# Kernel optimization log

Hardware: AMD Instinct MI355X
Metric: run time of the kernel (lower is better)

Reference implementation:

```python
import jax, jax.numpy as jnp
import numpy as np

L0, L1, L2 = 32, 16, 8          # multiplicities of 0e, 1o, 2e irreps
NS = 128                        # numscalars
NB = 64                         # numbasis
CUTOFF = 7.0
N_NODES = 50000
N_EDGES = 400000
N_GRAPH = 32
NODE_DIM = L0 + 3 * L1 + 5 * L2  # 120


def setup_inputs() -> dict:
    key = jax.random.key(0)
    ks = jax.random.split(key, 16)
    return {
        "nodes": jax.random.normal(ks[0], (N_NODES, NODE_DIM), jnp.float32),
        "edge_index": jax.random.randint(ks[1], (2, N_EDGES), 0, N_NODES),
        "graph_batch": jnp.sort(jax.random.randint(ks[2], (N_NODES,), 0, N_GRAPH)),
        "cell": jax.random.normal(ks[3], (N_GRAPH, 3, 3), jnp.float32),
        "edge_shift": jax.random.normal(ks[4], (N_EDGES, 3), jnp.float32),
        "pos": jax.random.normal(ks[5], (N_NODES, 3), jnp.float32),
        # FullyConnectedTensorProduct weights: one uvw block per (l,l)->0e path
        "W0": jax.random.normal(ks[6], (L0, L0, NS), jnp.float32),
        "W1": jax.random.normal(ks[7], (L1, L1, NS), jnp.float32),
        "W2": jax.random.normal(ks[8], (L2, L2, NS), jnp.float32),
        "ln_g": jnp.ones((NS,), jnp.float32),
        "ln_b": jnp.zeros((NS,), jnp.float32),
        "df_w1": jax.random.normal(ks[9], (NB, 128), jnp.float32) / np.sqrt(NB).astype(np.float32),
        "df_b1": jnp.zeros((128,), jnp.float32),
        "df_w2": jax.random.normal(ks[10], (128, NS), jnp.float32) / np.sqrt(128.0).astype(np.float32),
        "df_b2": jnp.zeros((NS,), jnp.float32),
        "mlp_w1": jax.random.normal(ks[11], (NS, 512), jnp.float32) / np.sqrt(NS).astype(np.float32),
        "mlp_b1": jnp.zeros((512,), jnp.float32),
        "mlp_w2": jax.random.normal(ks[12], (512, 1), jnp.float32) / np.sqrt(512.0).astype(np.float32),
        "mlp_b2": jnp.zeros((1,), jnp.float32),
    }


def _split_irreps(x):
    # x: [E, L0 + 3*L1 + 5*L2] -> scalar / vector / rank-2 blocks
    a = x[:, :L0]                                   # [E, L0]    0e
    b = x[:, L0:L0 + 3 * L1].reshape(-1, L1, 3)     # [E, L1, 3] 1o
    c = x[:, L0 + 3 * L1:].reshape(-1, L2, 5)       # [E, L2, 5] 2e
    return a, b, c


def _tensor_product(x1, x2, W0, W1, W2):
    # e3nn FullyConnectedTensorProduct to {NS}x0e: only (l,l)->0 paths survive.
    # Real-basis wigner_3j(l,l,0) = I / sqrt(2l+1); 'element' path norm with
    # scalar output gives alpha = 1 / (L0^2 + L1^2 + L2^2) shared by all paths.
    a1, b1, c1 = _split_irreps(x1)
    a2, b2, c2 = _split_irreps(x2)
    alpha = 1.0 / np.sqrt(float(L0 * L0 + L1 * L1 + L2 * L2))
    out = (jnp.einsum('eu,ev,uvw->ew', a1, a2, W0)
           + jnp.einsum('eum,evm,uvw->ew', b1, b2, W1) * (1.0 / np.sqrt(3.0))
           + jnp.einsum('eum,evm,uvw->ew', c1, c2, W2) * (1.0 / np.sqrt(5.0)))
    return jnp.asarray(alpha, out.dtype) * out


def reference(nodes, edge_index, graph_batch, cell, edge_shift, pos,
              W0, W1, W2, ln_g, ln_b, df_w1, df_b1, df_w2, df_b2,
              mlp_w1, mlp_b1, mlp_w2, mlp_b2):
    src, dst = edge_index[0], edge_index[1]
    bcell = cell[graph_batch[src]]                            # [E,3,3]
    tvec = jnp.einsum('ei,eij->ej', edge_shift, bcell)        # [E,3]
    radvec = pos[dst] - pos[src] + tvec
    dist = jnp.linalg.norm(radvec, axis=1, keepdims=True)     # [E,1]

    mixed = _tensor_product(nodes[src], nodes[dst], W0, W1, W2)  # [E,NS]
    mu = jnp.mean(mixed, axis=-1, keepdims=True)
    var = jnp.mean((mixed - mu) ** 2, axis=-1, keepdims=True)
    mixednorm = (mixed - mu) / jnp.sqrt(var + 1e-5) * ln_g + ln_b

    # RadialEmbedding: Gaussian RBF * cosine envelope with hard cutoff
    offset = jnp.linspace(0.0, CUTOFF, NB).astype(dist.dtype)
    width = CUTOFF / (NB - 1)
    coeff = -0.5 / (width * width)
    rbf = jnp.exp(coeff * (dist - offset[None, :]) ** 2)      # [E,NB]
    env = 0.5 * (jnp.cos(dist * jnp.pi / CUTOFF) + 1.0)
    env = env * (dist < CUTOFF).astype(dist.dtype)            # [E,1]
    demb = rbf * env

    dfilter = jax.nn.silu(demb @ df_w1 + df_b1) @ df_w2 + df_b2  # [E,NS]
    regulated = mixednorm * dfilter
    out = jax.nn.silu(regulated @ mlp_w1 + mlp_b1) @ mlp_w2 + mlp_b2  # [E,1]
    return out
```

## Files before the change

kernel.cpp:

```cpp
#include <hip/hip_runtime.h>
#include <hip/hip_bf16.h>
#include <math.h>

typedef unsigned short ushort_t;
typedef short short8 __attribute__((ext_vector_type(8)));
typedef float f32x4 __attribute__((ext_vector_type(4)));

#define E_TOTAL 400000
#define ET 64
#define NTHR 512
#define NODE_D 120
#define ASTR 36
#define BCSTR 92

#define ALPHA 0.0272772362793f
#define S_L1  0.57735026918962f
#define S_L2  0.44721359549996f

#define WS_WF1 172032
#define WS_WF2 180224
#define WS_WM1 196608
#define WS_TOTAL 262144

__device__ __forceinline__ ushort_t f2b(float f) {
    unsigned int b = __float_as_uint(f);
    b += 0x7FFFu + ((b >> 16) & 1u);
    return (ushort_t)(b >> 16);
}
__device__ __forceinline__ unsigned int f2b2(float a, float b) {
    __hip_bfloat162 h = __float22bfloat162_rn(make_float2(a, b));
    union { __hip_bfloat162 h2; unsigned int u; } cv; cv.h2 = h;
    return cv.u;
}
__device__ __forceinline__ float silu_f(float x) { return x / (1.0f + __expf(-x)); }

__global__ __launch_bounds__(256) void prep_weights(
    const float* __restrict__ W0, const float* __restrict__ W1, const float* __restrict__ W2,
    const float* __restrict__ df_w1, const float* __restrict__ df_w2,
    const float* __restrict__ mlp_w1, ushort_t* __restrict__ ws)
{
    const int i = blockIdx.x * 256 + threadIdx.x;
    if (i >= WS_TOTAL) return;
    float v;
    if (i < WS_WF1) {
        const int r = i;
        const int kt = r >> 12, nt = (r >> 9) & 7, l = (r >> 3) & 63, jj = r & 7;
        const int k = kt * 32 + ((l >> 4) << 3) + jj;
        const int n = nt * 16 + (l & 15);
        if (k < 1024)      v = W0[k * 128 + n] * ALPHA;
        else if (k < 1280) v = W1[(k - 1024) * 128 + n] * (ALPHA * S_L1);
        else               v = W2[(k - 1280) * 128 + n] * (ALPHA * S_L2);
    } else if (i < WS_WF2) {
        const int r = i - WS_WF1;
        const int kt = r >> 12, nt = (r >> 9) & 7, l = (r >> 3) & 63, jj = r & 7;
        v = df_w1[(kt * 32 + ((l >> 4) << 3) + jj) * 128 + nt * 16 + (l & 15)];
    } else if (i < WS_WM1) {
        const int r = i - WS_WF2;
        const int kt = r >> 12, nt = (r >> 9) & 7, l = (r >> 3) & 63, jj = r & 7;
        v = df_w2[(kt * 32 + ((l >> 4) << 3) + jj) * 128 + nt * 16 + (l & 15)];
    } else {
        const int r = i - WS_WM1;
        const int kt = r >> 14, nt = (r >> 9) & 31, l = (r >> 3) & 63, jj = r & 7;
        v = mlp_w1[(kt * 32 + ((l >> 4) << 3) + jj) * 512 + nt * 16 + (l & 15)];
    }
    ws[i] = f2b(v);
}

__global__ __launch_bounds__(NTHR, 4) void fused_edge_kernel(
    const float* __restrict__ nodes, const int* __restrict__ edge_index,
    const int* __restrict__ graph_batch, const float* __restrict__ cell,
    const float* __restrict__ edge_shift, const float* __restrict__ pos,
    const float* __restrict__ ln_g, const float* __restrict__ ln_b,
    const float* __restrict__ df_b1, const float* __restrict__ df_b2,
    const float* __restrict__ mlp_b1, const float* __restrict__ mlp_w2,
    const float* __restrict__ mlp_b2,
    const ushort_t* __restrict__ wsp, float* __restrict__ out)
{
    __shared__ __align__(16) ushort_t Pf[8 * 4 * 64 * 8];
    __shared__ __align__(16) char Xb[47104];
    __shared__ float dist_s[ET];
    __shared__ int sidx[ET], didx[ET];
    __shared__ float mu_s[ET], rstd_s[ET];

    float* xa1 = (float*)Xb;
    float* xa2 = xa1 + ET * ASTR;
    float* bc1 = (float*)Xb;
    float* bc2 = bc1 + ET * BCSTR;
    ushort_t* h1F  = (ushort_t*)Xb;
    ushort_t* regF = h1F + 8192;
    float* red1 = (float*)(Xb + 32768);
    float* red2 = (float*)(Xb + 36864);
    ushort_t* dembF = Pf + 4096;

    const int tid = threadIdx.x;
    const int e0g = blockIdx.x * ET;
    const int wave = tid >> 6, lane = tid & 63;
    const int lr = lane & 15, lg = lane >> 4;
    const int er = tid & 15, kg = (tid >> 4) & 3, w = tid >> 6;

    if (tid < ET) {
        const int e = e0g + tid;
        const int s = edge_index[e];
        const int d = edge_index[E_TOTAL + e];
        sidx[tid] = s; didx[tid] = d;
        const int g = graph_batch[s];
        const float* c = cell + g * 9;
        const float sx = edge_shift[e * 3], sy = edge_shift[e * 3 + 1], sz = edge_shift[e * 3 + 2];
        const float t0 = sx * c[0] + sy * c[3] + sz * c[6];
        const float t1 = sx * c[1] + sy * c[4] + sz * c[7];
        const float t2 = sx * c[2] + sy * c[5] + sz * c[8];
        const float r0 = pos[d * 3 + 0] - pos[s * 3 + 0] + t0;
        const float r1 = pos[d * 3 + 1] - pos[s * 3 + 1] + t1;
        const float r2 = pos[d * 3 + 2] - pos[s * 3 + 2] + t2;
        dist_s[tid] = sqrtf(r0 * r0 + r1 * r1 + r2 * r2);
    }
    __syncthreads();

    {
        const int e = tid >> 3, c = tid & 7;
        *(float4*)(xa1 + e * ASTR + c * 4) = *(const float4*)(nodes + (size_t)sidx[e] * NODE_D + c * 4);
        *(float4*)(xa2 + e * ASTR + c * 4) = *(const float4*)(nodes + (size_t)didx[e] * NODE_D + c * 4);
    }
    __syncthreads();

    const char* pA = (const char*)Pf + lane * 16;
    const short8* WT8 = (const short8*)wsp;
    const int bcol = tid;

    f32x4 acc[4] = {{0.f,0.f,0.f,0.f},{0.f,0.f,0.f,0.f},{0.f,0.f,0.f,0.f},{0.f,0.f,0.f,0.f}};

    float2 a2v[4][4];
#pragma unroll
    for (int h = 0; h < 4; ++h)
#pragma unroll
        for (int q = 0; q < 4; ++q)
            a2v[h][q] = *(const float2*)(xa2 + (h * 16 + er) * ASTR + kg * 8 + q * 2);

#pragma unroll 1
    for (int c4 = 0; c4 < 4; ++c4) {
#pragma unroll
        for (int h = 0; h < 4; ++h) {
            const float a1 = xa1[(h * 16 + er) * ASTR + c4 * 8 + w];
            uint4 o;
            o.x = f2b2(a1 * a2v[h][0].x, a1 * a2v[h][0].y);
            o.y = f2b2(a1 * a2v[h][1].x, a1 * a2v[h][1].y);
            o.z = f2b2(a1 * a2v[h][2].x, a1 * a2v[h][2].y);
            o.w = f2b2(a1 * a2v[h][3].x, a1 * a2v[h][3].y);
            *(uint4*)(Pf + ((w * 4 + h) * 64 + kg * 16 + er) * 8) = o;
        }
        __syncthreads();
#pragma unroll 2
        for (int kt = 0; kt < 8; ++kt) {
            const short8 b = WT8[(c4 * 8 + kt) * 512 + bcol];
#pragma unroll
            for (int h = 0; h < 4; ++h) {
                const short8 a = *(const short8*)(pA + (kt * 4 + h) * 1024);
                acc[h] = __builtin_amdgcn_mfma_f32_16x16x32_bf16(a, b, acc[h], 0, 0, 0);
            }
        }
        if (c4 == 3) {
            for (int i = tid; i < ET * 22; i += NTHR) {
                const int e = i / 22, c = i % 22;
                *(float4*)(bc1 + e * BCSTR + c * 4) =
                    *(const float4*)(nodes + (size_t)sidx[e] * NODE_D + 32 + c * 4);
            }
            for (int i = tid; i < ET * 22; i += NTHR) {
                const int e = i / 22, c = i % 22;
                *(float4*)(bc2 + e * BCSTR + c * 4) =
                    *(const float4*)(nodes + (size_t)didx[e] * NODE_D + 32 + c * 4);
            }
        }
        __syncthreads();
    }

    {
        const int u1 = 2 * w + (kg >> 1);
        const int vb = (kg & 1) * 8;
#pragma unroll
        for (int h = 0; h < 4; ++h) {
            const int e = h * 16 + er;
            const float* b1p = bc1 + e * BCSTR + 3 * u1;
            const float b1a = b1p[0], b1b = b1p[1], b1c = b1p[2];
            const float* b2b = bc2 + e * BCSTR + 3 * vb;
            float pr[8];
#pragma unroll
            for (int jj = 0; jj < 8; ++jj) {
                const float* b2p = b2b + 3 * jj;
                pr[jj] = b1a * b2p[0] + b1b * b2p[1] + b1c * b2p[2];
            }
            uint4 o;
            o.x = f2b2(pr[0], pr[1]); o.y = f2b2(pr[2], pr[3]);
            o.z = f2b2(pr[4], pr[5]); o.w = f2b2(pr[6], pr[7]);
            *(uint4*)(Pf + ((w * 4 + h) * 64 + kg * 16 + er) * 8) = o;
        }
    }
    __syncthreads();
#pragma unroll 2
    for (int kt = 0; kt < 8; ++kt) {
        const short8 b = WT8[(32 + kt) * 512 + bcol];
#pragma unroll
        for (int h = 0; h < 4; ++h) {
            const short8 a = *(const short8*)(pA + (kt * 4 + h) * 1024);
            acc[h] = __builtin_amdgcn_mfma_f32_16x16x32_bf16(a, b, acc[h], 0, 0, 0);
        }
    }
    __syncthreads();

    {
        const int ktl = w >> 2, h2 = w & 3;
        const int u2 = ktl * 4 + kg;
        const int e = h2 * 16 + er;
        const float* c1p = bc1 + e * BCSTR + 48 + 5 * u2;
        const float c1a = c1p[0], c1b = c1p[1], c1c = c1p[2], c1d = c1p[3], c1e = c1p[4];
        float pr[8];
#pragma unroll
        for (int jj = 0; jj < 8; ++jj) {
            const float* c2p = bc2 + e * BCSTR + 48 + 5 * jj;
            pr[jj] = c1a * c2p[0] + c1b * c2p[1] + c1c * c2p[2] + c1d * c2p[3] + c1e * c2p[4];
        }
        uint4 o;
        o.x = f2b2(pr[0], pr[1]); o.y = f2b2(pr[2], pr[3]);
        o.z = f2b2(pr[4], pr[5]); o.w = f2b2(pr[6], pr[7]);
        *(uint4*)(Pf + ((ktl * 4 + h2) * 64 + kg * 16 + er) * 8) = o;
    }
    __syncthreads();
#pragma unroll
    for (int kt = 0; kt < 2; ++kt) {
        const short8 b = WT8[(40 + kt) * 512 + bcol];
#pragma unroll
        for (int h = 0; h < 4; ++h) {
            const short8 a = *(const short8*)(pA + (kt * 4 + h) * 1024);
            acc[h] = __builtin_amdgcn_mfma_f32_16x16x32_bf16(a, b, acc[h], 0, 0, 0);
        }
    }
    for (int i = tid; i < ET * 64; i += NTHR) {
        const int e = i >> 6, k = i & 63;
        const float d = dist_s[e];
        const float t = d - (7.0f / 63.0f) * (float)k;
        const float rbf = __expf(-40.5f * t * t);
        const float env = (d < 7.0f) ? (0.5f * (__cosf(d * (3.14159265358979f / 7.0f)) + 1.0f)) : 0.0f;
        const int ktl = k >> 5, kgd = (k >> 3) & 3, jj = k & 7, half = e >> 4, row = e & 15;
        dembF[((ktl * 4 + half) * 64 + kgd * 16 + row) * 8 + jj] = f2b(rbf * env);
    }
    __syncthreads();

    {
        f32x4 f[4] = {{0.f,0.f,0.f,0.f},{0.f,0.f,0.f,0.f},{0.f,0.f,0.f,0.f},{0.f,0.f,0.f,0.f}};
        const char* dA = (const char*)dembF + lane * 16;
#pragma unroll
        for (int kt = 0; kt < 2; ++kt) {
            const short8 b = WT8[WS_WF1 / 8 + kt * 512 + bcol];
#pragma unroll
            for (int h = 0; h < 4; ++h) {
                const short8 a = *(const short8*)(dA + (kt * 4 + h) * 1024);
                f[h] = __builtin_amdgcn_mfma_f32_16x16x32_bf16(a, b, f[h], 0, 0, 0);
            }
        }
        const int n = wave * 16 + lr;
        const float bb = df_b1[n];
        const int ktl = n >> 5, kg2 = (n >> 3) & 3, jjn = n & 7;
#pragma unroll
        for (int h = 0; h < 4; ++h)
#pragma unroll
            for (int r = 0; r < 4; ++r)
                h1F[((ktl * 4 + h) * 64 + kg2 * 16 + lg * 4 + r) * 8 + jjn] = f2b(silu_f(f[h][r] + bb));
    }
    __syncthreads();

    f32x4 d[4] = {{0.f,0.f,0.f,0.f},{0.f,0.f,0.f,0.f},{0.f,0.f,0.f,0.f},{0.f,0.f,0.f,0.f}};
    {
        const char* hA = (const char*)h1F + lane * 16;
#pragma unroll
        for (int kt = 0; kt < 4; ++kt) {
            const short8 b = WT8[WS_WF2 / 8 + kt * 512 + bcol];
#pragma unroll
            for (int h = 0; h < 4; ++h) {
                const short8 a = *(const short8*)(hA + (kt * 4 + h) * 1024);
                d[h] = __builtin_amdgcn_mfma_f32_16x16x32_bf16(a, b, d[h], 0, 0, 0);
            }
        }
        const int n = wave * 16 + lr;
        const float b2v = df_b2[n];
#pragma unroll
        for (int h = 0; h < 4; ++h)
#pragma unroll
            for (int r = 0; r < 4; ++r) d[h][r] += b2v;
    }
#pragma unroll
    for (int h = 0; h < 4; ++h) {
#pragma unroll
        for (int r = 0; r < 4; ++r) {
            const float v = acc[h][r];
            float s1 = v, s2 = v * v;
            s1 += __shfl_xor(s1, 1);  s2 += __shfl_xor(s2, 1);
            s1 += __shfl_xor(s1, 2);  s2 += __shfl_xor(s2, 2);
            s1 += __shfl_xor(s1, 4);  s2 += __shfl_xor(s2, 4);
            s1 += __shfl_xor(s1, 8);  s2 += __shfl_xor(s2, 8);
            if (lr == 0) {
                const int idx = ((wave * 4 + h) * 4 + lg) * 4 + r;
                red1[idx] = s1;
                red1[512 + idx] = s2;
            }
        }
    }
    __syncthreads();
    if (tid < ET) {
        const int h = tid >> 4, g = (tid >> 2) & 3, r = tid & 3;
        float s1 = 0.f, s2 = 0.f;
#pragma unroll
        for (int ww = 0; ww < 8; ++ww) {
            const int idx = ((ww * 4 + h) * 4 + g) * 4 + r;
            s1 += red1[idx];
            s2 += red1[512 + idx];
        }
        const float mu = s1 * (1.0f / 128.0f);
        const float var = s2 * (1.0f / 128.0f) - mu * mu;
        mu_s[tid] = mu;
        rstd_s[tid] = rsqrtf(var + 1e-5f);
    }
    __syncthreads();

    {
        const int n = wave * 16 + lr;
        const float gv = ln_g[n], bv = ln_b[n];
        const int ktl = n >> 5, kg2 = (n >> 3) & 3, jjn = n & 7;
#pragma unroll
        for (int h = 0; h < 4; ++h) {
#pragma unroll
            for (int r = 0; r < 4; ++r) {
                const int row = lg * 4 + r, e = h * 16 + row;
                const float ln = (acc[h][r] - mu_s[e]) * rstd_s[e] * gv + bv;
                regF[((ktl * 4 + h) * 64 + kg2 * 16 + row) * 8 + jjn] = f2b(ln * d[h][r]);
            }
        }
    }
    __syncthreads();

    {
        f32x4 m[4][4];
#pragma unroll
        for (int q = 0; q < 4; ++q)
#pragma unroll
            for (int h = 0; h < 4; ++h) m[q][h] = (f32x4){0.f,0.f,0.f,0.f};
        const char* rA = (const char*)regF + lane * 16;
#pragma unroll
        for (int kt = 0; kt < 4; ++kt) {
            short8 a[4];
#pragma unroll
            for (int h = 0; h < 4; ++h)
                a[h] = *(const short8*)(rA + (kt * 4 + h) * 1024);
            const int base = WS_WM1 / 8 + kt * 2048 + wave * 256 + lane;
#pragma unroll
            for (int q = 0; q < 4; ++q) {
                const short8 b = WT8[base + q * 64];
#pragma unroll
                for (int h = 0; h < 4; ++h)
                    m[q][h] = __builtin_amdgcn_mfma_f32_16x16x32_bf16(a[h], b, m[q][h], 0, 0, 0);
            }
        }
        float po[4][4];
#pragma unroll
        for (int h = 0; h < 4; ++h)
#pragma unroll
            for (int r = 0; r < 4; ++r) po[h][r] = 0.f;
#pragma unroll
        for (int q = 0; q < 4; ++q) {
            const int n = (wave * 4 + q) * 16 + lr;
            const float b1v = mlp_b1[n];
            const float w2v = mlp_w2[n];
#pragma unroll
            for (int h = 0; h < 4; ++h)
#pragma unroll
                for (int r = 0; r < 4; ++r)
                    po[h][r] += silu_f(m[q][h][r] + b1v) * w2v;
        }
#pragma unroll
        for (int h = 0; h < 4; ++h) {
#pragma unroll
            for (int r = 0; r < 4; ++r) {
                float a = po[h][r];
                a += __shfl_xor(a, 1);
                a += __shfl_xor(a, 2);
                a += __shfl_xor(a, 4);
                a += __shfl_xor(a, 8);
                if (lr == 0) red2[((wave * 4 + h) * 4 + lg) * 4 + r] = a;
            }
        }
    }
    __syncthreads();
    if (tid < ET) {
        const int h = tid >> 4, g = (tid >> 2) & 3, r = tid & 3;
        float s = 0.f;
#pragma unroll
        for (int ww = 0; ww < 8; ++ww)
            s += red2[((ww * 4 + h) * 4 + g) * 4 + r];
        out[e0g + tid] = s + mlp_b2[0];
    }
}

extern "C" void kernel_launch(void* const* d_in, const int* in_sizes, int n_in,
                              void* d_out, int out_size, void* d_ws, size_t ws_size,
                              hipStream_t stream) {
    const float* nodes      = (const float*)d_in[0];
    const int*   edge_index = (const int*)  d_in[1];
    const int*   graph_b    = (const int*)  d_in[2];
    const float* cell       = (const float*)d_in[3];
    const float* edge_shift = (const float*)d_in[4];
    const float* pos        = (const float*)d_in[5];
    const float* W0         = (const float*)d_in[6];
    const float* W1         = (const float*)d_in[7];
    const float* W2         = (const float*)d_in[8];
    const float* ln_g       = (const float*)d_in[9];
    const float* ln_b       = (const float*)d_in[10];
    const float* df_w1      = (const float*)d_in[11];
    const float* df_b1      = (const float*)d_in[12];
    const float* df_w2      = (const float*)d_in[13];
    const float* df_b2      = (const float*)d_in[14];
    const float* mlp_w1     = (const float*)d_in[15];
    const float* mlp_b1     = (const float*)d_in[16];
    const float* mlp_w2     = (const float*)d_in[17];
    const float* mlp_b2     = (const float*)d_in[18];
    float* out = (float*)d_out;
    ushort_t* ws = (ushort_t*)d_ws;

    hipLaunchKernelGGL(prep_weights, dim3((WS_TOTAL + 255) / 256), dim3(256), 0, stream,
                       W0, W1, W2, df_w1, df_w2, mlp_w1, ws);

    const int E = in_sizes[1] / 2;
    const int grid = E / ET;
    hipLaunchKernelGGL(fused_edge_kernel, dim3(grid), dim3(NTHR), 0, stream,
                       nodes, edge_index, graph_b, cell, edge_shift, pos,
                       ln_g, ln_b, df_b1, df_b2, mlp_b1, mlp_w2, mlp_b2,
                       ws, out);
}
```

Before: 458.2 us.

## Build tensor-product MFMA A-fragments in registers and raise occupancy target

The outer-product A operands for the 0e, 1o and 2e paths are now built directly in registers per lane and fed straight to MFMA, so they no longer go through the shared Pf staging buffer and its per-chunk barriers. The shared arena is re-laid out into separate compact B and C blocks that are loaded earlier, overlapping with the 0e chunks. The final MLP accumulates in two halves to cut live accumulator registers, and launch bounds ask for 6 blocks per CU. In exchange each lane recomputes its products redundantly, and the lower register budget risks spills.

```diff
diff --git a/kernel.cpp b/kernel.cpp
--- a/kernel.cpp
+++ b/kernel.cpp
@@ -11,7 +11,8 @@
 #define NTHR 512
 #define NODE_D 120
 #define ASTR 36
-#define BCSTR 92
+#define BSTR 48
+#define CSTR 44
 
 #define ALPHA 0.0272772362793f
 #define S_L1  0.57735026918962f
@@ -66,7 +67,7 @@
     ws[i] = f2b(v);
 }
 
-__global__ __launch_bounds__(NTHR, 4) void fused_edge_kernel(
+__global__ __launch_bounds__(NTHR, 6) void fused_edge_kernel(
     const float* __restrict__ nodes, const int* __restrict__ edge_index,
     const int* __restrict__ graph_batch, const float* __restrict__ cell,
     const float* __restrict__ edge_shift, const float* __restrict__ pos,
@@ -76,27 +77,28 @@
     const float* __restrict__ mlp_b2,
     const ushort_t* __restrict__ wsp, float* __restrict__ out)
 {
-    __shared__ __align__(16) ushort_t Pf[8 * 4 * 64 * 8];
-    __shared__ __align__(16) char Xb[47104];
+    __shared__ __align__(16) char Ar[47104];
     __shared__ float dist_s[ET];
     __shared__ int sidx[ET], didx[ET];
     __shared__ float mu_s[ET], rstd_s[ET];
 
-    float* xa1 = (float*)Xb;
-    float* xa2 = xa1 + ET * ASTR;
-    float* bc1 = (float*)Xb;
-    float* bc2 = bc1 + ET * BCSTR;
-    ushort_t* h1F  = (ushort_t*)Xb;
-    ushort_t* regF = h1F + 8192;
-    float* red1 = (float*)(Xb + 32768);
-    float* red2 = (float*)(Xb + 36864);
-    ushort_t* dembF = Pf + 4096;
+    float* xa1 = (float*)(Ar + 24576);
+    float* xa2 = (float*)(Ar + 33792);
+    float* b1s = (float*)Ar;
+    float* b2s = (float*)(Ar + 12288);
+    float* c1s = (float*)(Ar + 24576);
+    float* c2s = (float*)(Ar + 35840);
+    ushort_t* h1F  = (ushort_t*)Ar;
+    ushort_t* regF = (ushort_t*)Ar + 8192;
+    float* red1 = (float*)(Ar + 32768);
+    float* red2 = (float*)(Ar + 36864);
+    ushort_t* dembF = (ushort_t*)(Ar + 38912);
 
     const int tid = threadIdx.x;
     const int e0g = blockIdx.x * ET;
     const int wave = tid >> 6, lane = tid & 63;
     const int lr = lane & 15, lg = lane >> 4;
-    const int er = tid & 15, kg = (tid >> 4) & 3, w = tid >> 6;
+    const int er = lane & 15, kg = lane >> 4;
 
     if (tid < ET) {
         const int e = e0g + tid;
@@ -123,7 +125,6 @@
     }
     __syncthreads();
 
-    const char* pA = (const char*)Pf + lane * 16;
     const short8* WT8 = (const short8*)wsp;
     const int bcol = tid;
 
@@ -138,101 +139,108 @@
 
 #pragma unroll 1
     for (int c4 = 0; c4 < 4; ++c4) {
-#pragma unroll
+        if (c4 == 1) {
+            for (int i = tid; i < 64 * 16; i += NTHR) {
+                const int e = i >> 4, c = i & 15;
+                if (c < 12) {
+                    *(float4*)(b1s + e * BSTR + c * 4) =
+                        *(const float4*)(nodes + (size_t)sidx[e] * NODE_D + 32 + c * 4);
+                    *(float4*)(b2s + e * BSTR + c * 4) =
+                        *(const float4*)(nodes + (size_t)didx[e] * NODE_D + 32 + c * 4);
+                }
+            }
+        }
+#pragma unroll 2
         for (int h = 0; h < 4; ++h) {
-            const float a1 = xa1[(h * 16 + er) * ASTR + c4 * 8 + w];
-            uint4 o;
-            o.x = f2b2(a1 * a2v[h][0].x, a1 * a2v[h][0].y);
-            o.y = f2b2(a1 * a2v[h][1].x, a1 * a2v[h][1].y);
-            o.z = f2b2(a1 * a2v[h][2].x, a1 * a2v[h][2].y);
-            o.w = f2b2(a1 * a2v[h][3].x, a1 * a2v[h][3].y);
-            *(uint4*)(Pf + ((w * 4 + h) * 64 + kg * 16 + er) * 8) = o;
-        }
-        __syncthreads();
+            const float* a1p = xa1 + (h * 16 + er) * ASTR + c4 * 8;
+            const f32x4 a1a = *(const f32x4*)a1p;
+            const f32x4 a1b = *(const f32x4*)(a1p + 4);
+            float a1arr[8] = {a1a[0],a1a[1],a1a[2],a1a[3],a1b[0],a1b[1],a1b[2],a1b[3]};
+#pragma unroll
+            for (int k8 = 0; k8 < 8; ++k8) {
+                const float a1 = a1arr[k8];
+                union { uint4 u; short8 s; } fr;
+                fr.u.x = f2b2(a1 * a2v[h][0].x, a1 * a2v[h][0].y);
+                fr.u.y = f2b2(a1 * a2v[h][1].x, a1 * a2v[h][1].y);
+                fr.u.z = f2b2(a1 * a2v[h][2].x, a1 * a2v[h][2].y);
+                fr.u.w = f2b2(a1 * a2v[h][3].x, a1 * a2v[h][3].y);
+                const short8 b = WT8[(c4 * 8 + k8) * 512 + bcol];
+                acc[h] = __builtin_amdgcn_mfma_f32_16x16x32_bf16(fr.s, b, acc[h], 0, 0, 0);
+            }
+        }
+    }
+    __syncthreads();
+
+#pragma unroll 1
+    for (int h = 0; h < 4; ++h) {
+        if (h == 1) {
+            for (int i = tid; i < 64 * 16; i += NTHR) {
+                const int e = i >> 4, c = i & 15;
+                if (c < 10) {
+                    *(float4*)(c1s + e * CSTR + c * 4) =
+                        *(const float4*)(nodes + (size_t)sidx[e] * NODE_D + 80 + c * 4);
+                    *(float4*)(c2s + e * CSTR + c * 4) =
+                        *(const float4*)(nodes + (size_t)didx[e] * NODE_D + 80 + c * 4);
+                }
+            }
+        }
+        const int e = h * 16 + er;
+        const float* b2p = b2s + e * BSTR + 3 * ((kg & 1) * 8);
+        f32x4 b2q[6];
+#pragma unroll
+        for (int q = 0; q < 6; ++q) b2q[q] = *(const f32x4*)(b2p + q * 4);
+#pragma unroll
+        for (int ktl = 0; ktl < 8; ++ktl) {
+            const int u = 2 * ktl + (kg >> 1);
+            const float* b1p = b1s + e * BSTR + 3 * u;
+            const float ba = b1p[0], bb = b1p[1], bc = b1p[2];
+            float pr[8];
+#pragma unroll
+            for (int jj = 0; jj < 8; ++jj) {
+                const int t = 3 * jj;
+                pr[jj] = ba * b2q[t >> 2][t & 3] + bb * b2q[(t + 1) >> 2][(t + 1) & 3]
+                       + bc * b2q[(t + 2) >> 2][(t + 2) & 3];
+            }
+            union { uint4 u4; short8 s; } fr;
+            fr.u4.x = f2b2(pr[0], pr[1]); fr.u4.y = f2b2(pr[2], pr[3]);
+            fr.u4.z = f2b2(pr[4], pr[5]); fr.u4.w = f2b2(pr[6], pr[7]);
+            const short8 b = WT8[(32 + ktl) * 512 + bcol];
+            acc[h] = __builtin_amdgcn_mfma_f32_16x16x32_bf16(fr.s, b, acc[h], 0, 0, 0);
+        }
+    }
+    __syncthreads();
+
 #pragma unroll 2
-        for (int kt = 0; kt < 8; ++kt) {
-            const short8 b = WT8[(c4 * 8 + kt) * 512 + bcol];
-#pragma unroll
-            for (int h = 0; h < 4; ++h) {
-                const short8 a = *(const short8*)(pA + (kt * 4 + h) * 1024);
-                acc[h] = __builtin_amdgcn_mfma_f32_16x16x32_bf16(a, b, acc[h], 0, 0, 0);
-            }
-        }
-        if (c4 == 3) {
-            for (int i = tid; i < ET * 22; i += NTHR) {
-                const int e = i / 22, c = i % 22;
-                *(float4*)(bc1 + e * BCSTR + c * 4) =
-                    *(const float4*)(nodes + (size_t)sidx[e] * NODE_D + 32 + c * 4);
-            }
-            for (int i = tid; i < ET * 22; i += NTHR) {
-                const int e = i / 22, c = i % 22;
-                *(float4*)(bc2 + e * BCSTR + c * 4) =
-                    *(const float4*)(nodes + (size_t)didx[e] * NODE_D + 32 + c * 4);
-            }
-        }
-        __syncthreads();
-    }
-
-    {
-        const int u1 = 2 * w + (kg >> 1);
-        const int vb = (kg & 1) * 8;
-#pragma unroll
-        for (int h = 0; h < 4; ++h) {
-            const int e = h * 16 + er;
-            const float* b1p = bc1 + e * BCSTR + 3 * u1;
-            const float b1a = b1p[0], b1b = b1p[1], b1c = b1p[2];
-            const float* b2b = bc2 + e * BCSTR + 3 * vb;
+    for (int h = 0; h < 4; ++h) {
+        const int e = h * 16 + er;
+        const float* c2p = c2s + e * CSTR;
+        f32x4 c2q[10];
+#pragma unroll
+        for (int q = 0; q < 10; ++q) c2q[q] = *(const f32x4*)(c2p + q * 4);
+#pragma unroll
+        for (int ktl = 0; ktl < 2; ++ktl) {
+            const int u = ktl * 4 + kg;
+            const float* c1p = c1s + e * CSTR + 5 * u;
+            const float ca = c1p[0], cb = c1p[1], cc = c1p[2], cd = c1p[3], ce = c1p[4];
             float pr[8];
 #pragma unroll
             for (int jj = 0; jj < 8; ++jj) {
-                const float* b2p = b2b + 3 * jj;
-                pr[jj] = b1a * b2p[0] + b1b * b2p[1] + b1c * b2p[2];
-            }
-            uint4 o;
-            o.x = f2b2(pr[0], pr[1]); o.y = f2b2(pr[2], pr[3]);
-            o.z = f2b2(pr[4], pr[5]); o.w = f2b2(pr[6], pr[7]);
-            *(uint4*)(Pf + ((w * 4 + h) * 64 + kg * 16 + er) * 8) = o;
-        }
-    }
-    __syncthreads();
-#pragma unroll 2
-    for (int kt = 0; kt < 8; ++kt) {
-        const short8 b = WT8[(32 + kt) * 512 + bcol];
-#pragma unroll
-        for (int h = 0; h < 4; ++h) {
-            const short8 a = *(const short8*)(pA + (kt * 4 + h) * 1024);
-            acc[h] = __builtin_amdgcn_mfma_f32_16x16x32_bf16(a, b, acc[h], 0, 0, 0);
-        }
-    }
-    __syncthreads();
-
-    {
-        const int ktl = w >> 2, h2 = w & 3;
-        const int u2 = ktl * 4 + kg;
-        const int e = h2 * 16 + er;
-        const float* c1p = bc1 + e * BCSTR + 48 + 5 * u2;
-        const float c1a = c1p[0], c1b = c1p[1], c1c = c1p[2], c1d = c1p[3], c1e = c1p[4];
-        float pr[8];
-#pragma unroll
-        for (int jj = 0; jj < 8; ++jj) {
-            const float* c2p = bc2 + e * BCSTR + 48 + 5 * jj;
-            pr[jj] = c1a * c2p[0] + c1b * c2p[1] + c1c * c2p[2] + c1d * c2p[3] + c1e * c2p[4];
-        }
-        uint4 o;
-        o.x = f2b2(pr[0], pr[1]); o.y = f2b2(pr[2], pr[3]);
-        o.z = f2b2(pr[4], pr[5]); o.w = f2b2(pr[6], pr[7]);
-        *(uint4*)(Pf + ((ktl * 4 + h2) * 64 + kg * 16 + er) * 8) = o;
-    }
-    __syncthreads();
-#pragma unroll
-    for (int kt = 0; kt < 2; ++kt) {
-        const short8 b = WT8[(40 + kt) * 512 + bcol];
-#pragma unroll
-        for (int h = 0; h < 4; ++h) {
-            const short8 a = *(const short8*)(pA + (kt * 4 + h) * 1024);
-            acc[h] = __builtin_amdgcn_mfma_f32_16x16x32_bf16(a, b, acc[h], 0, 0, 0);
-        }
-    }
+                const int t = 5 * jj;
+                pr[jj] = ca * c2q[t >> 2][t & 3]
+                       + cb * c2q[(t + 1) >> 2][(t + 1) & 3]
+                       + cc * c2q[(t + 2) >> 2][(t + 2) & 3]
+                       + cd * c2q[(t + 3) >> 2][(t + 3) & 3]
+                       + ce * c2q[(t + 4) >> 2][(t + 4) & 3];
+            }
+            union { uint4 u4; short8 s; } fr;
+            fr.u4.x = f2b2(pr[0], pr[1]); fr.u4.y = f2b2(pr[2], pr[3]);
+            fr.u4.z = f2b2(pr[4], pr[5]); fr.u4.w = f2b2(pr[6], pr[7]);
+            const short8 b = WT8[(40 + ktl) * 512 + bcol];
+            acc[h] = __builtin_amdgcn_mfma_f32_16x16x32_bf16(fr.s, b, acc[h], 0, 0, 0);
+        }
+    }
+    __syncthreads();
+
     for (int i = tid; i < ET * 64; i += NTHR) {
         const int e = i >> 6, k = i & 63;
         const float d = dist_s[e];
@@ -337,42 +345,45 @@
     __syncthreads();
 
     {
-        f32x4 m[4][4];
-#pragma unroll
-        for (int q = 0; q < 4; ++q)
-#pragma unroll
-            for (int h = 0; h < 4; ++h) m[q][h] = (f32x4){0.f,0.f,0.f,0.f};
+        float po[4][4];
+#pragma unroll
+        for (int h = 0; h < 4; ++h)
+#pragma unroll
+            for (int r = 0; r < 4; ++r) po[h][r] = 0.f;
         const char* rA = (const char*)regF + lane * 16;
-#pragma unroll
-        for (int kt = 0; kt < 4; ++kt) {
-            short8 a[4];
-#pragma unroll
-            for (int h = 0; h < 4; ++h)
-                a[h] = *(const short8*)(rA + (kt * 4 + h) * 1024);
-            const int base = WS_WM1 / 8 + kt * 2048 + wave * 256 + lane;
-#pragma unroll
-            for (int q = 0; q < 4; ++q) {
-                const short8 b = WT8[base + q * 64];
+#pragma unroll 1
+        for (int qp = 0; qp < 2; ++qp) {
+            f32x4 m[2][4];
+#pragma unroll
+            for (int qq = 0; qq < 2; ++qq)
+#pragma unroll
+                for (int h = 0; h < 4; ++h) m[qq][h] = (f32x4){0.f,0.f,0.f,0.f};
+#pragma unroll
+            for (int kt = 0; kt < 4; ++kt) {
+                short8 a[4];
 #pragma unroll
                 for (int h = 0; h < 4; ++h)
-                    m[q][h] = __builtin_amdgcn_mfma_f32_16x16x32_bf16(a[h], b, m[q][h], 0, 0, 0);
-            }
-        }
-        float po[4][4];
-#pragma unroll
-        for (int h = 0; h < 4; ++h)
-#pragma unroll
-            for (int r = 0; r < 4; ++r) po[h][r] = 0.f;
-#pragma unroll
-        for (int q = 0; q < 4; ++q) {
-            const int n = (wave * 4 + q) * 16 + lr;
-            const float b1v = mlp_b1[n];
-            const float w2v = mlp_w2[n];
-#pragma unroll
-            for (int h = 0; h < 4; ++h)
-#pragma unroll
-                for (int r = 0; r < 4; ++r)
-                    po[h][r] += silu_f(m[q][h][r] + b1v) * w2v;
+                    a[h] = *(const short8*)(rA + (kt * 4 + h) * 1024);
+                const int base = WS_WM1 / 8 + kt * 2048 + wave * 256 + lane + qp * 128;
+#pragma unroll
+                for (int qq = 0; qq < 2; ++qq) {
+                    const short8 b = WT8[base + qq * 64];
+#pragma unroll
+                    for (int h = 0; h < 4; ++h)
+                        m[qq][h] = __builtin_amdgcn_mfma_f32_16x16x32_bf16(a[h], b, m[qq][h], 0, 0, 0);
+                }
+            }
+#pragma unroll
+            for (int qq = 0; qq < 2; ++qq) {
+                const int n = (wave * 4 + qp * 2 + qq) * 16 + lr;
+                const float b1v = mlp_b1[n];
+                const float w2v = mlp_w2[n];
+#pragma unroll
+                for (int h = 0; h < 4; ++h)
+#pragma unroll
+                    for (int r = 0; r < 4; ++r)
+                        po[h][r] += silu_f(m[qq][h][r] + b1v) * w2v;
+            }
         }
 #pragma unroll
         for (int h = 0; h < 4; ++h) {
```

Result: slower. 1.737 ms (+279.2%).
